# Optimization experiments

Hardware: AMD Instinct MI355X
Metric: run time of the kernel (lower is better)

## Reference

```python
import jax, jax.numpy as jnp
import numpy as np

B, N, D, DIM = 64, 512, 128, 128
NEG_INF = -1e9


def setup_inputs() -> dict:
    key = jax.random.key(0)
    k1, k2, k3, k4 = jax.random.split(key, 4)
    atom_query = jax.random.normal(k1, (B, N, D), dtype=jnp.float32)
    # binary atom-presence mask, broadcastable over feature dim
    mask = jax.random.randint(k2, (B, N, 1), 0, 2).astype(jnp.float32)
    s = 1.0 / np.sqrt(D)
    Wq = jax.random.normal(k3, (D, DIM), dtype=jnp.float32) * s
    Wk = jax.random.normal(k4, (D, DIM), dtype=jnp.float32) * s
    bq = jnp.zeros((DIM,), dtype=jnp.float32)
    bk = jnp.zeros((DIM,), dtype=jnp.float32)
    return {"atom_query": atom_query, "mask": mask, "Wq": Wq, "bq": bq, "Wk": Wk, "bk": bk}


def reference(atom_query, mask, Wq, bq, Wk, bk):
    # projections
    q = atom_query @ Wq + bq              # [B, N, dim]
    k = atom_query @ Wk + bk              # [B, N, dim]
    mq = mask * q                          # masked query
    mk = mask * k                          # masked key

    # energy[b,i,j] = mk[b,i] . mq[b,j], with diagonal zeroed, then summed over j.
    # sum_j energy[b,i,j] = mk[b,i] . (sum_j mq[b,j]) - mk[b,i] . mq[b,i]
    # (identical math to materializing the [B,N,N] energy and reducing)
    q_sum = mq.sum(axis=1)                                   # [B, dim]
    agg = jnp.einsum('bnd,bd->bn', mk, q_sum) - (mk * mq).sum(-1)  # [B, N]
    agg = agg[:, :, None] * mask                             # [B, N, 1]

    # euclidean normalize over atom axis (tf.linalg.normalize, axis=1)
    nrm = jnp.sqrt(jnp.sum(agg * agg, axis=1, keepdims=True))
    agg = agg / nrm

    # masked softmax over atoms
    agg = agg + (1.0 - mask) * NEG_INF
    attn = jax.nn.softmax(agg, axis=1)                       # [B, N, 1]

    # v_proj=False, kq_proj=True -> values are the key projection
    context = jnp.sum(mask * attn * k, axis=1)               # [B, dim]
    return attn, context
```

## Files before the change

kernel.cpp:

```cpp
#include <hip/hip_runtime.h>
#include <math.h>

#define NB 64
#define NN 512
#define ND 128

typedef __attribute__((ext_vector_type(8))) short short8;
typedef __attribute__((ext_vector_type(4))) float f32x4;

#define KVB_OFF   0
#define QK_OFF    (NB*NN*ND/2)
#define QSUMP_OFF (QK_OFF + NB*NN)

__device__ inline unsigned short f2bf(float x) {
    unsigned int u = __float_as_uint(x);
    return (unsigned short)((u + 0x7FFFu + ((u >> 16) & 1u)) >> 16);
}
__device__ inline float bf2f(unsigned short u) {
    return __uint_as_float(((unsigned int)u) << 16);
}

__global__ __launch_bounds__(256, 1) void proj_mfma(
    const float* __restrict__ aq, const float* __restrict__ mask,
    const float* __restrict__ Wq, const float* __restrict__ bq,
    const float* __restrict__ Wk, const float* __restrict__ bk,
    unsigned short* __restrict__ kvb, float* __restrict__ qk,
    float* __restrict__ qsum_part)
{
    __shared__ __align__(16) unsigned char sbuf[34816];
    unsigned short (*wst)[132] = (unsigned short (*)[132])sbuf;
    unsigned short (*ast)[136] = (unsigned short (*)[136])sbuf;
    __shared__ float mask_lds[128];
    __shared__ float qk_part[4][128];

    const int b    = blockIdx.x >> 2;
    const int m0   = (blockIdx.x & 3) << 7;
    const int t    = threadIdx.x;
    const int w    = t >> 6, lane = t & 63;
    const int quad = lane >> 4, l16 = lane & 15;

    short8 bfr[4][4];

    #pragma unroll
    for (int s = 0; s < 2; s++) {
        const float* Wsrc = s ? Wk : Wq;
        if (s) __syncthreads();
        {
            const float4* src = (const float4*)Wsrc;
            #pragma unroll
            for (int i = 0; i < 16; i++) {
                const int idx = t + 256*i;
                const int row = idx >> 5, c4 = idx & 31;
                const float4 v = src[idx];
                ushort4 o;
                o.x = f2bf(v.x); o.y = f2bf(v.y); o.z = f2bf(v.z); o.w = f2bf(v.w);
                *(ushort4*)&wst[row][c4*4] = o;
            }
        }
        __syncthreads();
        #pragma unroll
        for (int nt = 0; nt < 2; nt++) {
            const int col = w*32 + nt*16 + l16;
            #pragma unroll
            for (int kc = 0; kc < 4; kc++) {
                short8 v;
                #pragma unroll
                for (int j = 0; j < 8; j++)
                    v[j] = (short)wst[kc*32 + quad*8 + j][col];
                bfr[s*2 + nt][kc] = v;
            }
        }
    }
    __syncthreads();

    {
        const float4* src = (const float4*)(aq + ((size_t)b*NN + m0)*ND);
        #pragma unroll
        for (int i = 0; i < 16; i++) {
            const int idx = t + 256*i;
            const int row = idx >> 5, c4 = idx & 31;
            const float4 v = src[idx];
            ushort4 o;
            o.x = f2bf(v.x); o.y = f2bf(v.y); o.z = f2bf(v.z); o.w = f2bf(v.w);
            *(ushort4*)&ast[row][c4*4] = o;
        }
        if (t < 128) mask_lds[t] = mask[b*NN + m0 + t];
    }
    __syncthreads();

    f32x4 acc[8][4];
    #pragma unroll
    for (int m = 0; m < 8; m++)
        #pragma unroll
        for (int nt = 0; nt < 4; nt++)
            acc[m][nt] = (f32x4){0.f, 0.f, 0.f, 0.f};

    #pragma unroll
    for (int m = 0; m < 8; m++) {
        short8 afr[4];
        #pragma unroll
        for (int kc = 0; kc < 4; kc++)
            afr[kc] = *(const short8*)&ast[m*16 + l16][kc*32 + quad*8];
        #pragma unroll
        for (int nt = 0; nt < 4; nt++)
            #pragma unroll
            for (int kc = 0; kc < 4; kc++)
                acc[m][nt] = __builtin_amdgcn_mfma_f32_16x16x32_bf16(
                    afr[kc], bfr[nt][kc], acc[m][nt], 0, 0, 0);
    }

    float bv[4];
    #pragma unroll
    for (int nt = 0; nt < 2; nt++) bv[nt] = bq[w*32 + nt*16 + l16];
    #pragma unroll
    for (int nt = 2; nt < 4; nt++) bv[nt] = bk[w*32 + (nt-2)*16 + l16];
    #pragma unroll
    for (int m = 0; m < 8; m++)
        #pragma unroll
        for (int nt = 0; nt < 4; nt++)
            #pragma unroll
            for (int r = 0; r < 4; r++)
                acc[m][nt][r] += bv[nt];

    #pragma unroll
    for (int m = 0; m < 8; m++)
        #pragma unroll
        for (int r = 0; r < 4; r++) {
            const size_t row = (size_t)b*NN + m0 + m*16 + quad*4 + r;
            kvb[row*ND + w*32 + l16]      = f2bf(acc[m][2][r]);
            kvb[row*ND + w*32 + 16 + l16] = f2bf(acc[m][3][r]);
        }

    #pragma unroll
    for (int m = 0; m < 8; m++) {
        float p[4];
        #pragma unroll
        for (int r = 0; r < 4; r++)
            p[r] = acc[m][0][r]*acc[m][2][r] + acc[m][1][r]*acc[m][3][r];
        #pragma unroll
        for (int off = 1; off <= 8; off <<= 1)
            #pragma unroll
            for (int r = 0; r < 4; r++)
                p[r] += __shfl_xor(p[r], off);
        if (l16 == 0)
            #pragma unroll
            for (int r = 0; r < 4; r++)
                qk_part[w][m*16 + quad*4 + r] = p[r];
    }

    {
        float s0 = 0.f, s1 = 0.f;
        #pragma unroll
        for (int m = 0; m < 8; m++)
            #pragma unroll
            for (int r = 0; r < 4; r++) {
                const float mk = mask_lds[m*16 + quad*4 + r];
                s0 += mk * acc[m][0][r];
                s1 += mk * acc[m][1][r];
            }
        s0 += __shfl_xor(s0, 16); s0 += __shfl_xor(s0, 32);
        s1 += __shfl_xor(s1, 16); s1 += __shfl_xor(s1, 32);
        if (quad == 0) {
            const int slot = blockIdx.x * ND;
            qsum_part[slot + w*32 + l16]      = s0;
            qsum_part[slot + w*32 + 16 + l16] = s1;
        }
    }

    __syncthreads();
    if (t < 128)
        qk[(size_t)b*NN + m0 + t] =
            qk_part[0][t] + qk_part[1][t] + qk_part[2][t] + qk_part[3][t];
}

__global__ __launch_bounds__(512) void fused_attn(
    const float* __restrict__ mask, const unsigned short* __restrict__ kvb,
    const float* __restrict__ qk, const float* __restrict__ qsum_part,
    float* __restrict__ out_attn, float* __restrict__ out_ctx)
{
    __shared__ float qs[128];
    __shared__ float mask_s[512];
    __shared__ float agg_s[512];
    __shared__ float red[16];
    __shared__ float bc2[2];
    __shared__ float zred[8];
    __shared__ float zbc;
    __shared__ float ctx_part[32][33];

    const int b  = blockIdx.x >> 2;
    const int cg = blockIdx.x & 3;
    const int t = threadIdx.x, w = t >> 6, lane = t & 63;
    const size_t rowbase = (size_t)b * NN;

    if (t < 128)
        qs[t] = qsum_part[(b*4 + 0)*ND + t] + qsum_part[(b*4 + 1)*ND + t]
              + qsum_part[(b*4 + 2)*ND + t] + qsum_part[(b*4 + 3)*ND + t];
    mask_s[t] = mask[rowbase + t];
    __syncthreads();

    const int h = lane & 15, quad = lane >> 4;
    float qsf[8];
    #pragma unroll
    for (int j = 0; j < 8; j++) qsf[j] = qs[h*8 + j];

    for (int i0 = 0; i0 < 64; i0 += 4) {
        const int n = w*64 + i0 + quad;
        const short8 kr = *(const short8*)(kvb + (rowbase + n)*ND + h*8);
        float p = 0.f;
        #pragma unroll
        for (int j = 0; j < 8; j++)
            p += bf2f((unsigned short)kr[j]) * qsf[j];
        #pragma unroll
        for (int off = 1; off <= 8; off <<= 1) p += __shfl_xor(p, off);
        if (h == 0)
            agg_s[n] = mask_s[n] * (p - qk[rowbase + n]);
    }
    __syncthreads();

    const float v  = agg_s[t];
    const bool um  = mask_s[t] != 0.f;
    float sq = v * v;
    float mx = um ? v : -3.0e38f;
    #pragma unroll
    for (int off = 1; off <= 32; off <<= 1) {
        sq += __shfl_xor(sq, off);
        mx = fmaxf(mx, __shfl_xor(mx, off));
    }
    if (lane == 0) { red[w] = sq; red[8 + w] = mx; }
    __syncthreads();
    if (t == 0) {
        float s = 0.f, m = -3.0e38f;
        #pragma unroll
        for (int i = 0; i < 8; i++) { s += red[i]; m = fmaxf(m, red[8 + i]); }
        bc2[0] = sqrtf(s);
        bc2[1] = m;
    }
    __syncthreads();
    const float nrm = bc2[0];
    const float M   = bc2[1];

    const float e = um ? expf((v - M) / nrm) : 0.f;
    float z = e;
    #pragma unroll
    for (int off = 1; off <= 32; off <<= 1) z += __shfl_xor(z, off);
    if (lane == 0) zred[w] = z;
    agg_s[t] = e;
    __syncthreads();
    if (t == 0) {
        float s = 0.f;
        #pragma unroll
        for (int i = 0; i < 8; i++) s += zred[i];
        zbc = s;
    }
    __syncthreads();
    const float Z = zbc;
    if (cg == 0) out_attn[rowbase + t] = e / Z;

    const int c2  = (t & 15) * 2;
    const int col = cg*32 + c2;
    const int rg  = t >> 4;
    float a0 = 0.f, a1 = 0.f;
    for (int n = rg; n < NN; n += 32) {
        const ushort2 kk = *(const ushort2*)(kvb + (rowbase + n)*ND + col);
        const float ev = agg_s[n];
        a0 += ev * bf2f(kk.x);
        a1 += ev * bf2f(kk.y);
    }
    ctx_part[rg][c2]     = a0;
    ctx_part[rg][c2 + 1] = a1;
    __syncthreads();
    if (t < 32) {
        float s = 0.f;
        #pragma unroll
        for (int i = 0; i < 32; i++) s += ctx_part[i][t];
        out_ctx[(size_t)b*ND + cg*32 + t] = s / Z;
    }
}

extern "C" void kernel_launch(void* const* d_in, const int* in_sizes, int n_in,
                              void* d_out, int out_size, void* d_ws, size_t ws_size,
                              hipStream_t stream)
{
    const float* aq   = (const float*)d_in[0];
    const float* mask = (const float*)d_in[1];
    const float* Wq   = (const float*)d_in[2];
    const float* bq   = (const float*)d_in[3];
    const float* Wk   = (const float*)d_in[4];
    const float* bk   = (const float*)d_in[5];

    float* ws = (float*)d_ws;
    unsigned short* kvb       = (unsigned short*)(ws + KVB_OFF);
    float*          qk        = ws + QK_OFF;
    float*          qsum_part = ws + QSUMP_OFF;

    float* out_attn = (float*)d_out;
    float* out_ctx  = (float*)d_out + NB*NN;

    proj_mfma<<<dim3(256), dim3(256), 0, stream>>>(aq, mask, Wq, bq, Wk, bk,
                                                   kvb, qk, qsum_part);
    fused_attn<<<dim3(256), dim3(512), 0, stream>>>(mask, kvb, qk, qsum_part,
                                                    out_attn, out_ctx);
}
```

Measured before the change: 96.88 us.

## Fuse projection and attention into one per-batch kernel keeping K in LDS

Merges the two kernels into a single kernel with one 512-thread block per batch. The block projects the batch's atoms in 32-row chunks with a register prefetch of the next chunk, keeps the bf16 key projection in shared memory, and then runs the normalize, softmax and context reduction on-chip. This removes the workspace round trip for K, qk and the partial query sums, plus the second launch. The cost is a grid of only 64 blocks on a GPU with many more compute units, so each batch is processed serially inside one block with a sync-heavy chunk loop.

```diff
diff --git a/kernel.cpp b/kernel.cpp
--- a/kernel.cpp
+++ b/kernel.cpp
@@ -8,10 +8,6 @@
 typedef __attribute__((ext_vector_type(8))) short short8;
 typedef __attribute__((ext_vector_type(4))) float f32x4;
 
-#define KVB_OFF   0
-#define QK_OFF    (NB*NN*ND/2)
-#define QSUMP_OFF (QK_OFF + NB*NN)
-
 __device__ inline unsigned short f2bf(float x) {
     unsigned int u = __float_as_uint(x);
     return (unsigned short)((u + 0x7FFFu + ((u >> 16) & 1u)) >> 16);
@@ -20,200 +16,191 @@
     return __uint_as_float(((unsigned int)u) << 16);
 }
 
-__global__ __launch_bounds__(256, 1) void proj_mfma(
+__global__ __launch_bounds__(512, 1) void ga_one(
     const float* __restrict__ aq, const float* __restrict__ mask,
     const float* __restrict__ Wq, const float* __restrict__ bq,
     const float* __restrict__ Wk, const float* __restrict__ bk,
-    unsigned short* __restrict__ kvb, float* __restrict__ qk,
-    float* __restrict__ qsum_part)
+    float* __restrict__ out_attn, float* __restrict__ out_ctx)
 {
-    __shared__ __align__(16) unsigned char sbuf[34816];
-    unsigned short (*wst)[132] = (unsigned short (*)[132])sbuf;
-    unsigned short (*ast)[136] = (unsigned short (*)[136])sbuf;
-    __shared__ float mask_lds[128];
-    __shared__ float qk_part[4][128];
-
-    const int b    = blockIdx.x >> 2;
-    const int m0   = (blockIdx.x & 3) << 7;
+    __shared__ __align__(16) unsigned char kv_raw[512 * 136 * 2];
+    __shared__ __align__(16) unsigned char ab_raw[32 * 136 * 2];
+    __shared__ float mask_s[512];
+    __shared__ float agg_s[512];
+    __shared__ float qkp[4][512];
+    __shared__ float qs[128];
+    __shared__ float red2[16];
+    __shared__ float bcast[4];
+
+    unsigned short (*kv)[136]  = (unsigned short (*)[136])kv_raw;
+    unsigned short (*wst)[268] = (unsigned short (*)[268])kv_raw;
+    unsigned short (*ab)[136]  = (unsigned short (*)[136])ab_raw;
+    float (*ctx_part)[128]     = (float (*)[128])ab_raw;
+
+    const int b    = blockIdx.x;
     const int t    = threadIdx.x;
     const int w    = t >> 6, lane = t & 63;
     const int quad = lane >> 4, l16 = lane & 15;
-
-    short8 bfr[4][4];
-
-    #pragma unroll
-    for (int s = 0; s < 2; s++) {
-        const float* Wsrc = s ? Wk : Wq;
-        if (s) __syncthreads();
-        {
-            const float4* src = (const float4*)Wsrc;
-            #pragma unroll
-            for (int i = 0; i < 16; i++) {
-                const int idx = t + 256*i;
-                const int row = idx >> 5, c4 = idx & 31;
-                const float4 v = src[idx];
-                ushort4 o;
-                o.x = f2bf(v.x); o.y = f2bf(v.y); o.z = f2bf(v.z); o.w = f2bf(v.w);
-                *(ushort4*)&wst[row][c4*4] = o;
-            }
-        }
-        __syncthreads();
-        #pragma unroll
-        for (int nt = 0; nt < 2; nt++) {
-            const int col = w*32 + nt*16 + l16;
+    const bool isq = (w < 4);
+    const int cb   = (w & 3) * 32;
+
+    {
+        const float4* srcq = (const float4*)Wq;
+        const float4* srck = (const float4*)Wk;
+        #pragma unroll
+        for (int i = 0; i < 8; i++) {
+            const int idx = t + 512*i;
+            const int k = idx >> 5, c4 = idx & 31;
+            float4 v = srcq[idx];
+            ushort4 o;
+            o.x = f2bf(v.x); o.y = f2bf(v.y); o.z = f2bf(v.z); o.w = f2bf(v.w);
+            *(ushort4*)&wst[k][c4*4] = o;
+            v = srck[idx];
+            o.x = f2bf(v.x); o.y = f2bf(v.y); o.z = f2bf(v.z); o.w = f2bf(v.w);
+            *(ushort4*)&wst[k][128 + c4*4] = o;
+        }
+        mask_s[t] = mask[(size_t)b*NN + t];
+    }
+    __syncthreads();
+
+    short8 bfr[2][4];
+    {
+        const int colbase = cb + (isq ? 0 : 128);
+        #pragma unroll
+        for (int nt = 0; nt < 2; nt++)
             #pragma unroll
             for (int kc = 0; kc < 4; kc++) {
                 short8 v;
                 #pragma unroll
                 for (int j = 0; j < 8; j++)
-                    v[j] = (short)wst[kc*32 + quad*8 + j][col];
-                bfr[s*2 + nt][kc] = v;
+                    v[j] = (short)wst[kc*32 + quad*8 + j][colbase + nt*16 + l16];
+                bfr[nt][kc] = v;
             }
-        }
-    }
-    __syncthreads();
-
-    {
-        const float4* src = (const float4*)(aq + ((size_t)b*NN + m0)*ND);
-        #pragma unroll
-        for (int i = 0; i < 16; i++) {
-            const int idx = t + 256*i;
-            const int row = idx >> 5, c4 = idx & 31;
-            const float4 v = src[idx];
+    }
+    float bv[2];
+    #pragma unroll
+    for (int nt = 0; nt < 2; nt++)
+        bv[nt] = isq ? bq[cb + nt*16 + l16] : bk[cb + nt*16 + l16];
+    __syncthreads();
+
+    float s0 = 0.f, s1 = 0.f;
+
+    float4 pre0, pre1;
+    {
+        const float4* asrc = (const float4*)(aq + (size_t)b*NN*ND);
+        pre0 = asrc[t]; pre1 = asrc[t + 512];
+    }
+
+    for (int sc = 0; sc < 16; sc++) {
+        {
+            int idx = t, row = idx >> 5, c4 = idx & 31;
             ushort4 o;
-            o.x = f2bf(v.x); o.y = f2bf(v.y); o.z = f2bf(v.z); o.w = f2bf(v.w);
-            *(ushort4*)&ast[row][c4*4] = o;
-        }
-        if (t < 128) mask_lds[t] = mask[b*NN + m0 + t];
-    }
-    __syncthreads();
-
-    f32x4 acc[8][4];
-    #pragma unroll
-    for (int m = 0; m < 8; m++)
-        #pragma unroll
-        for (int nt = 0; nt < 4; nt++)
-            acc[m][nt] = (f32x4){0.f, 0.f, 0.f, 0.f};
-
-    #pragma unroll
-    for (int m = 0; m < 8; m++) {
-        short8 afr[4];
-        #pragma unroll
-        for (int kc = 0; kc < 4; kc++)
-            afr[kc] = *(const short8*)&ast[m*16 + l16][kc*32 + quad*8];
-        #pragma unroll
-        for (int nt = 0; nt < 4; nt++)
+            o.x = f2bf(pre0.x); o.y = f2bf(pre0.y); o.z = f2bf(pre0.z); o.w = f2bf(pre0.w);
+            *(ushort4*)&ab[row][c4*4] = o;
+            idx = t + 512; row = idx >> 5; c4 = idx & 31;
+            o.x = f2bf(pre1.x); o.y = f2bf(pre1.y); o.z = f2bf(pre1.z); o.w = f2bf(pre1.w);
+            *(ushort4*)&ab[row][c4*4] = o;
+        }
+        __syncthreads();
+        if (sc < 15) {
+            const float4* asrc = (const float4*)(aq + ((size_t)b*NN + (sc+1)*32)*ND);
+            pre0 = asrc[t]; pre1 = asrc[t + 512];
+        }
+
+        f32x4 acc[2][2];
+        #pragma unroll
+        for (int m = 0; m < 2; m++)
+            #pragma unroll
+            for (int nt = 0; nt < 2; nt++)
+                acc[m][nt] = (f32x4){0.f, 0.f, 0.f, 0.f};
+
+        #pragma unroll
+        for (int m = 0; m < 2; m++) {
+            short8 afr[4];
             #pragma unroll
             for (int kc = 0; kc < 4; kc++)
-                acc[m][nt] = __builtin_amdgcn_mfma_f32_16x16x32_bf16(
-                    afr[kc], bfr[nt][kc], acc[m][nt], 0, 0, 0);
-    }
-
-    float bv[4];
-    #pragma unroll
-    for (int nt = 0; nt < 2; nt++) bv[nt] = bq[w*32 + nt*16 + l16];
-    #pragma unroll
-    for (int nt = 2; nt < 4; nt++) bv[nt] = bk[w*32 + (nt-2)*16 + l16];
-    #pragma unroll
-    for (int m = 0; m < 8; m++)
-        #pragma unroll
-        for (int nt = 0; nt < 4; nt++)
-            #pragma unroll
-            for (int r = 0; r < 4; r++)
-                acc[m][nt][r] += bv[nt];
-
-    #pragma unroll
-    for (int m = 0; m < 8; m++)
-        #pragma unroll
-        for (int r = 0; r < 4; r++) {
-            const size_t row = (size_t)b*NN + m0 + m*16 + quad*4 + r;
-            kvb[row*ND + w*32 + l16]      = f2bf(acc[m][2][r]);
-            kvb[row*ND + w*32 + 16 + l16] = f2bf(acc[m][3][r]);
-        }
-
-    #pragma unroll
-    for (int m = 0; m < 8; m++) {
-        float p[4];
-        #pragma unroll
-        for (int r = 0; r < 4; r++)
-            p[r] = acc[m][0][r]*acc[m][2][r] + acc[m][1][r]*acc[m][3][r];
-        #pragma unroll
-        for (int off = 1; off <= 8; off <<= 1)
-            #pragma unroll
-            for (int r = 0; r < 4; r++)
-                p[r] += __shfl_xor(p[r], off);
-        if (l16 == 0)
-            #pragma unroll
-            for (int r = 0; r < 4; r++)
-                qk_part[w][m*16 + quad*4 + r] = p[r];
-    }
-
-    {
-        float s0 = 0.f, s1 = 0.f;
-        #pragma unroll
-        for (int m = 0; m < 8; m++)
-            #pragma unroll
-            for (int r = 0; r < 4; r++) {
-                const float mk = mask_lds[m*16 + quad*4 + r];
-                s0 += mk * acc[m][0][r];
-                s1 += mk * acc[m][1][r];
+                afr[kc] = *(const short8*)&ab[m*16 + l16][kc*32 + quad*8];
+            #pragma unroll
+            for (int nt = 0; nt < 2; nt++)
+                #pragma unroll
+                for (int kc = 0; kc < 4; kc++)
+                    acc[m][nt] = __builtin_amdgcn_mfma_f32_16x16x32_bf16(
+                        afr[kc], bfr[nt][kc], acc[m][nt], 0, 0, 0);
+        }
+        #pragma unroll
+        for (int m = 0; m < 2; m++)
+            #pragma unroll
+            for (int nt = 0; nt < 2; nt++)
+                #pragma unroll
+                for (int r = 0; r < 4; r++)
+                    acc[m][nt][r] += bv[nt];
+
+        if (!isq) {
+            #pragma unroll
+            for (int m = 0; m < 2; m++)
+                #pragma unroll
+                for (int r = 0; r < 4; r++) {
+                    const int row = sc*32 + m*16 + quad*4 + r;
+                    kv[row][cb + l16]      = f2bf(acc[m][0][r]);
+                    kv[row][cb + 16 + l16] = f2bf(acc[m][1][r]);
+                }
+        }
+        __syncthreads();
+
+        if (isq) {
+            #pragma unroll
+            for (int m = 0; m < 2; m++) {
+                float p[4];
+                #pragma unroll
+                for (int r = 0; r < 4; r++) {
+                    const int row = sc*32 + m*16 + quad*4 + r;
+                    p[r] = acc[m][0][r]*bf2f(kv[row][cb + l16])
+                         + acc[m][1][r]*bf2f(kv[row][cb + 16 + l16]);
+                }
+                #pragma unroll
+                for (int off = 1; off <= 8; off <<= 1)
+                    #pragma unroll
+                    for (int r = 0; r < 4; r++)
+                        p[r] += __shfl_xor(p[r], off);
+                if (l16 == 0)
+                    #pragma unroll
+                    for (int r = 0; r < 4; r++)
+                        qkp[w][sc*32 + m*16 + quad*4 + r] = p[r];
+                #pragma unroll
+                for (int r = 0; r < 4; r++) {
+                    const int row = sc*32 + m*16 + quad*4 + r;
+                    const float mk = mask_s[row];
+                    s0 += mk * acc[m][0][r];
+                    s1 += mk * acc[m][1][r];
+                }
             }
+        }
+    }
+
+    if (isq) {
         s0 += __shfl_xor(s0, 16); s0 += __shfl_xor(s0, 32);
         s1 += __shfl_xor(s1, 16); s1 += __shfl_xor(s1, 32);
-        if (quad == 0) {
-            const int slot = blockIdx.x * ND;
-            qsum_part[slot + w*32 + l16]      = s0;
-            qsum_part[slot + w*32 + 16 + l16] = s1;
-        }
-    }
-
-    __syncthreads();
-    if (t < 128)
-        qk[(size_t)b*NN + m0 + t] =
-            qk_part[0][t] + qk_part[1][t] + qk_part[2][t] + qk_part[3][t];
-}
-
-__global__ __launch_bounds__(512) void fused_attn(
-    const float* __restrict__ mask, const unsigned short* __restrict__ kvb,
-    const float* __restrict__ qk, const float* __restrict__ qsum_part,
-    float* __restrict__ out_attn, float* __restrict__ out_ctx)
-{
-    __shared__ float qs[128];
-    __shared__ float mask_s[512];
-    __shared__ float agg_s[512];
-    __shared__ float red[16];
-    __shared__ float bc2[2];
-    __shared__ float zred[8];
-    __shared__ float zbc;
-    __shared__ float ctx_part[32][33];
-
-    const int b  = blockIdx.x >> 2;
-    const int cg = blockIdx.x & 3;
-    const int t = threadIdx.x, w = t >> 6, lane = t & 63;
-    const size_t rowbase = (size_t)b * NN;
-
-    if (t < 128)
-        qs[t] = qsum_part[(b*4 + 0)*ND + t] + qsum_part[(b*4 + 1)*ND + t]
-              + qsum_part[(b*4 + 2)*ND + t] + qsum_part[(b*4 + 3)*ND + t];
-    mask_s[t] = mask[rowbase + t];
-    __syncthreads();
-
-    const int h = lane & 15, quad = lane >> 4;
-    float qsf[8];
-    #pragma unroll
-    for (int j = 0; j < 8; j++) qsf[j] = qs[h*8 + j];
-
-    for (int i0 = 0; i0 < 64; i0 += 4) {
-        const int n = w*64 + i0 + quad;
-        const short8 kr = *(const short8*)(kvb + (rowbase + n)*ND + h*8);
-        float p = 0.f;
-        #pragma unroll
-        for (int j = 0; j < 8; j++)
-            p += bf2f((unsigned short)kr[j]) * qsf[j];
-        #pragma unroll
-        for (int off = 1; off <= 8; off <<= 1) p += __shfl_xor(p, off);
-        if (h == 0)
-            agg_s[n] = mask_s[n] * (p - qk[rowbase + n]);
+        if (lane < 16) { qs[cb + lane] = s0; qs[cb + 16 + lane] = s1; }
+    }
+    __syncthreads();
+
+    {
+        float qsf[8];
+        #pragma unroll
+        for (int j = 0; j < 8; j++) qsf[j] = qs[l16*8 + j];
+        for (int i0 = 0; i0 < 64; i0 += 4) {
+            const int n = w*64 + i0 + quad;
+            const short8 kr = *(const short8*)&kv[n][l16*8];
+            float p = 0.f;
+            #pragma unroll
+            for (int j = 0; j < 8; j++)
+                p += bf2f((unsigned short)kr[j]) * qsf[j];
+            #pragma unroll
+            for (int off = 1; off <= 8; off <<= 1) p += __shfl_xor(p, off);
+            if (l16 == 0) {
+                const float qkv = qkp[0][n] + qkp[1][n] + qkp[2][n] + qkp[3][n];
+                agg_s[n] = mask_s[n] * (p - qkv);
+            }
+        }
     }
     __syncthreads();
 
@@ -226,55 +213,45 @@
         sq += __shfl_xor(sq, off);
         mx = fmaxf(mx, __shfl_xor(mx, off));
     }
-    if (lane == 0) { red[w] = sq; red[8 + w] = mx; }
+    if (lane == 0) { red2[w] = sq; red2[8 + w] = mx; }
     __syncthreads();
     if (t == 0) {
         float s = 0.f, m = -3.0e38f;
         #pragma unroll
-        for (int i = 0; i < 8; i++) { s += red[i]; m = fmaxf(m, red[8 + i]); }
-        bc2[0] = sqrtf(s);
-        bc2[1] = m;
-    }
-    __syncthreads();
-    const float nrm = bc2[0];
-    const float M   = bc2[1];
+        for (int i = 0; i < 8; i++) { s += red2[i]; m = fmaxf(m, red2[8 + i]); }
+        bcast[0] = sqrtf(s);
+        bcast[1] = m;
+    }
+    __syncthreads();
+    const float nrm = bcast[0];
+    const float M   = bcast[1];
 
     const float e = um ? expf((v - M) / nrm) : 0.f;
+    agg_s[t] = e;
     float z = e;
     #pragma unroll
     for (int off = 1; off <= 32; off <<= 1) z += __shfl_xor(z, off);
-    if (lane == 0) zred[w] = z;
-    agg_s[t] = e;
+    if (lane == 0) red2[w] = z;
     __syncthreads();
     if (t == 0) {
         float s = 0.f;
         #pragma unroll
-        for (int i = 0; i < 8; i++) s += zred[i];
-        zbc = s;
-    }
-    __syncthreads();
-    const float Z = zbc;
-    if (cg == 0) out_attn[rowbase + t] = e / Z;
-
-    const int c2  = (t & 15) * 2;
-    const int col = cg*32 + c2;
-    const int rg  = t >> 4;
-    float a0 = 0.f, a1 = 0.f;
-    for (int n = rg; n < NN; n += 32) {
-        const ushort2 kk = *(const ushort2*)(kvb + (rowbase + n)*ND + col);
-        const float ev = agg_s[n];
-        a0 += ev * bf2f(kk.x);
-        a1 += ev * bf2f(kk.y);
-    }
-    ctx_part[rg][c2]     = a0;
-    ctx_part[rg][c2 + 1] = a1;
-    __syncthreads();
-    if (t < 32) {
-        float s = 0.f;
-        #pragma unroll
-        for (int i = 0; i < 32; i++) s += ctx_part[i][t];
-        out_ctx[(size_t)b*ND + cg*32 + t] = s / Z;
-    }
+        for (int i = 0; i < 8; i++) s += red2[i];
+        bcast[2] = s;
+    }
+    __syncthreads();
+    const float Z = bcast[2];
+    out_attn[(size_t)b*NN + t] = e / Z;
+
+    const int col = t & 127, g = t >> 7;
+    float a = 0.f;
+    for (int n = g; n < NN; n += 4)
+        a += agg_s[n] * bf2f(kv[n][col]);
+    ctx_part[g][col] = a;
+    __syncthreads();
+    if (t < 128)
+        out_ctx[(size_t)b*ND + t] =
+            (ctx_part[0][t] + ctx_part[1][t] + ctx_part[2][t] + ctx_part[3][t]) / Z;
 }
 
 extern "C" void kernel_launch(void* const* d_in, const int* in_sizes, int n_in,
@@ -288,16 +265,9 @@
     const float* Wk   = (const float*)d_in[4];
     const float* bk   = (const float*)d_in[5];
 
-    float* ws = (float*)d_ws;
-    unsigned short* kvb       = (unsigned short*)(ws + KVB_OFF);
-    float*          qk        = ws + QK_OFF;
-    float*          qsum_part = ws + QSUMP_OFF;
-
     float* out_attn = (float*)d_out;
     float* out_ctx  = (float*)d_out + NB*NN;
 
-    proj_mfma<<<dim3(256), dim3(256), 0, stream>>>(aq, mask, Wq, bq, Wk, bk,
-                                                   kvb, qk, qsum_part);
-    fused_attn<<<dim3(256), dim3(512), 0, stream>>>(mask, kvb, qk, qsum_part,
-                                                    out_attn, out_ctx);
-}
+    ga_one<<<dim3(NB), dim3(512), 0, stream>>>(aq, mask, Wq, bq, Wk, bk,
+                                               out_attn, out_ctx);
+}
```

Measured after the change: 104.4 us. 7.7% more time.

## Fuse projection and attention kernels with per-batch inter-block flag sync

Applied to the files above, without the earlier changes.

Merges the projection kernel and the attention kernel into a single 256-block launch. The four blocks of each batch signal completion through release-stored flags in workspace and spin-wait on each other before running the normalize, softmax and context stage with 256 threads. Block indices are remapped so the four blocks of a batch land on the same XCD, which should keep the shared kvb data in one L2. This removes the second launch and the gap between kernels, but it needs all blocks to be resident at once. The flags are never reset, so on a later call the waits can pass before the other blocks of the batch have written their data.

```diff
diff --git a/kernel.cpp b/kernel.cpp
--- a/kernel.cpp
+++ b/kernel.cpp
@@ -4,6 +4,7 @@
 #define NB 64
 #define NN 512
 #define ND 128
+#define DONE_FLAG 0x1234ABCDu
 
 typedef __attribute__((ext_vector_type(8))) short short8;
 typedef __attribute__((ext_vector_type(4))) float f32x4;
@@ -11,6 +12,7 @@
 #define KVB_OFF   0
 #define QK_OFF    (NB*NN*ND/2)
 #define QSUMP_OFF (QK_OFF + NB*NN)
+#define FLAG_OFF  (QSUMP_OFF + NB*4*ND)
 
 __device__ inline unsigned short f2bf(float x) {
     unsigned int u = __float_as_uint(x);
@@ -20,27 +22,40 @@
     return __uint_as_float(((unsigned int)u) << 16);
 }
 
-__global__ __launch_bounds__(256, 1) void proj_mfma(
+__global__ __launch_bounds__(256, 1) void ga_fused(
     const float* __restrict__ aq, const float* __restrict__ mask,
     const float* __restrict__ Wq, const float* __restrict__ bq,
     const float* __restrict__ Wk, const float* __restrict__ bk,
     unsigned short* __restrict__ kvb, float* __restrict__ qk,
-    float* __restrict__ qsum_part)
+    float* __restrict__ qsum_part, unsigned int* __restrict__ flags,
+    float* __restrict__ out_attn, float* __restrict__ out_ctx)
 {
     __shared__ __align__(16) unsigned char sbuf[34816];
     unsigned short (*wst)[132] = (unsigned short (*)[132])sbuf;
     unsigned short (*ast)[136] = (unsigned short (*)[136])sbuf;
     __shared__ float mask_lds[128];
     __shared__ float qk_part[4][128];
-
-    const int b    = blockIdx.x >> 2;
-    const int m0   = (blockIdx.x & 3) << 7;
+    __shared__ float qs[128];
+    __shared__ float mask_s[512];
+    __shared__ float agg_s[512];
+    __shared__ float red[8];
+    __shared__ float bc2[2];
+    __shared__ float zred[4];
+    __shared__ float zbc;
+    __shared__ float ctx_part[16][33];
+
+    const int p    = blockIdx.x;
+    const int xcd  = p & 7, slot = p >> 3;
+    const int b    = ((slot >> 2) << 3) | xcd;
+    const int c    = slot & 3;
+    const int lb   = b*4 + c;
+    const int m0   = c << 7;
+
     const int t    = threadIdx.x;
     const int w    = t >> 6, lane = t & 63;
     const int quad = lane >> 4, l16 = lane & 15;
 
     short8 bfr[4][4];
-
     #pragma unroll
     for (int s = 0; s < 2; s++) {
         const float* Wsrc = s ? Wk : Wq;
@@ -133,19 +148,19 @@
 
     #pragma unroll
     for (int m = 0; m < 8; m++) {
-        float p[4];
+        float pr[4];
         #pragma unroll
         for (int r = 0; r < 4; r++)
-            p[r] = acc[m][0][r]*acc[m][2][r] + acc[m][1][r]*acc[m][3][r];
+            pr[r] = acc[m][0][r]*acc[m][2][r] + acc[m][1][r]*acc[m][3][r];
         #pragma unroll
         for (int off = 1; off <= 8; off <<= 1)
             #pragma unroll
             for (int r = 0; r < 4; r++)
-                p[r] += __shfl_xor(p[r], off);
+                pr[r] += __shfl_xor(pr[r], off);
         if (l16 == 0)
             #pragma unroll
             for (int r = 0; r < 4; r++)
-                qk_part[w][m*16 + quad*4 + r] = p[r];
+                qk_part[w][m*16 + quad*4 + r] = pr[r];
     }
 
     {
@@ -161,9 +176,9 @@
         s0 += __shfl_xor(s0, 16); s0 += __shfl_xor(s0, 32);
         s1 += __shfl_xor(s1, 16); s1 += __shfl_xor(s1, 32);
         if (quad == 0) {
-            const int slot = blockIdx.x * ND;
-            qsum_part[slot + w*32 + l16]      = s0;
-            qsum_part[slot + w*32 + 16 + l16] = s1;
+            const int slotq = lb * ND;
+            qsum_part[slotq + w*32 + l16]      = s0;
+            qsum_part[slotq + w*32 + 16 + l16] = s1;
         }
     }
 
@@ -171,67 +186,64 @@
     if (t < 128)
         qk[(size_t)b*NN + m0 + t] =
             qk_part[0][t] + qk_part[1][t] + qk_part[2][t] + qk_part[3][t];
-}
-
-__global__ __launch_bounds__(512) void fused_attn(
-    const float* __restrict__ mask, const unsigned short* __restrict__ kvb,
-    const float* __restrict__ qk, const float* __restrict__ qsum_part,
-    float* __restrict__ out_attn, float* __restrict__ out_ctx)
-{
-    __shared__ float qs[128];
-    __shared__ float mask_s[512];
-    __shared__ float agg_s[512];
-    __shared__ float red[16];
-    __shared__ float bc2[2];
-    __shared__ float zred[8];
-    __shared__ float zbc;
-    __shared__ float ctx_part[32][33];
-
-    const int b  = blockIdx.x >> 2;
-    const int cg = blockIdx.x & 3;
-    const int t = threadIdx.x, w = t >> 6, lane = t & 63;
+
+    __syncthreads();
+    __threadfence();
+    if (t == 0)
+        __hip_atomic_store(&flags[lb], DONE_FLAG, __ATOMIC_RELEASE,
+                           __HIP_MEMORY_SCOPE_AGENT);
+    if (t < 4) {
+        while (__hip_atomic_load(&flags[b*4 + t], __ATOMIC_RELAXED,
+                                 __HIP_MEMORY_SCOPE_AGENT) != DONE_FLAG)
+            __builtin_amdgcn_s_sleep(2);
+    }
+    __syncthreads();
+    __threadfence();
+
+    const int cg = c;
     const size_t rowbase = (size_t)b * NN;
 
     if (t < 128)
         qs[t] = qsum_part[(b*4 + 0)*ND + t] + qsum_part[(b*4 + 1)*ND + t]
               + qsum_part[(b*4 + 2)*ND + t] + qsum_part[(b*4 + 3)*ND + t];
-    mask_s[t] = mask[rowbase + t];
-    __syncthreads();
-
-    const int h = lane & 15, quad = lane >> 4;
-    float qsf[8];
-    #pragma unroll
-    for (int j = 0; j < 8; j++) qsf[j] = qs[h*8 + j];
-
-    for (int i0 = 0; i0 < 64; i0 += 4) {
-        const int n = w*64 + i0 + quad;
-        const short8 kr = *(const short8*)(kvb + (rowbase + n)*ND + h*8);
-        float p = 0.f;
-        #pragma unroll
-        for (int j = 0; j < 8; j++)
-            p += bf2f((unsigned short)kr[j]) * qsf[j];
-        #pragma unroll
-        for (int off = 1; off <= 8; off <<= 1) p += __shfl_xor(p, off);
-        if (h == 0)
-            agg_s[n] = mask_s[n] * (p - qk[rowbase + n]);
-    }
-    __syncthreads();
-
-    const float v  = agg_s[t];
-    const bool um  = mask_s[t] != 0.f;
-    float sq = v * v;
-    float mx = um ? v : -3.0e38f;
+    mask_s[t]       = mask[rowbase + t];
+    mask_s[t + 256] = mask[rowbase + t + 256];
+    __syncthreads();
+
+    {
+        float qsf[8];
+        #pragma unroll
+        for (int j = 0; j < 8; j++) qsf[j] = qs[l16*8 + j];
+        for (int i0 = 0; i0 < 128; i0 += 4) {
+            const int n = w*128 + i0 + quad;
+            const short8 kr = *(const short8*)(kvb + (rowbase + n)*ND + l16*8);
+            float pp = 0.f;
+            #pragma unroll
+            for (int j = 0; j < 8; j++)
+                pp += bf2f((unsigned short)kr[j]) * qsf[j];
+            #pragma unroll
+            for (int off = 1; off <= 8; off <<= 1) pp += __shfl_xor(pp, off);
+            if (l16 == 0)
+                agg_s[n] = mask_s[n] * (pp - qk[rowbase + n]);
+        }
+    }
+    __syncthreads();
+
+    const float v0 = agg_s[t], v1 = agg_s[t + 256];
+    const bool um0 = mask_s[t] != 0.f, um1 = mask_s[t + 256] != 0.f;
+    float sq = v0*v0 + v1*v1;
+    float mx = fmaxf(um0 ? v0 : -3.0e38f, um1 ? v1 : -3.0e38f);
     #pragma unroll
     for (int off = 1; off <= 32; off <<= 1) {
         sq += __shfl_xor(sq, off);
         mx = fmaxf(mx, __shfl_xor(mx, off));
     }
-    if (lane == 0) { red[w] = sq; red[8 + w] = mx; }
+    if (lane == 0) { red[w] = sq; red[4 + w] = mx; }
     __syncthreads();
     if (t == 0) {
         float s = 0.f, m = -3.0e38f;
         #pragma unroll
-        for (int i = 0; i < 8; i++) { s += red[i]; m = fmaxf(m, red[8 + i]); }
+        for (int i = 0; i < 4; i++) { s += red[i]; m = fmaxf(m, red[4 + i]); }
         bc2[0] = sqrtf(s);
         bc2[1] = m;
     }
@@ -239,28 +251,28 @@
     const float nrm = bc2[0];
     const float M   = bc2[1];
 
-    const float e = um ? expf((v - M) / nrm) : 0.f;
-    float z = e;
+    const float e0 = um0 ? expf((v0 - M) / nrm) : 0.f;
+    const float e1 = um1 ? expf((v1 - M) / nrm) : 0.f;
+    float z = e0 + e1;
     #pragma unroll
     for (int off = 1; off <= 32; off <<= 1) z += __shfl_xor(z, off);
     if (lane == 0) zred[w] = z;
-    agg_s[t] = e;
-    __syncthreads();
-    if (t == 0) {
-        float s = 0.f;
-        #pragma unroll
-        for (int i = 0; i < 8; i++) s += zred[i];
-        zbc = s;
-    }
+    agg_s[t] = e0;
+    agg_s[t + 256] = e1;
+    __syncthreads();
+    if (t == 0) zbc = zred[0] + zred[1] + zred[2] + zred[3];
     __syncthreads();
     const float Z = zbc;
-    if (cg == 0) out_attn[rowbase + t] = e / Z;
+    if (cg == 0) {
+        out_attn[rowbase + t]       = e0 / Z;
+        out_attn[rowbase + t + 256] = e1 / Z;
+    }
 
     const int c2  = (t & 15) * 2;
     const int col = cg*32 + c2;
     const int rg  = t >> 4;
     float a0 = 0.f, a1 = 0.f;
-    for (int n = rg; n < NN; n += 32) {
+    for (int n = rg; n < NN; n += 16) {
         const ushort2 kk = *(const ushort2*)(kvb + (rowbase + n)*ND + col);
         const float ev = agg_s[n];
         a0 += ev * bf2f(kk.x);
@@ -272,7 +284,7 @@
     if (t < 32) {
         float s = 0.f;
         #pragma unroll
-        for (int i = 0; i < 32; i++) s += ctx_part[i][t];
+        for (int i = 0; i < 16; i++) s += ctx_part[i][t];
         out_ctx[(size_t)b*ND + cg*32 + t] = s / Z;
     }
 }
@@ -292,12 +304,12 @@
     unsigned short* kvb       = (unsigned short*)(ws + KVB_OFF);
     float*          qk        = ws + QK_OFF;
     float*          qsum_part = ws + QSUMP_OFF;
+    unsigned int*   flags     = (unsigned int*)(ws + FLAG_OFF);
 
     float* out_attn = (float*)d_out;
     float* out_ctx  = (float*)d_out + NB*NN;
 
-    proj_mfma<<<dim3(256), dim3(256), 0, stream>>>(aq, mask, Wq, bq, Wk, bk,
-                                                   kvb, qk, qsum_part);
-    fused_attn<<<dim3(256), dim3(512), 0, stream>>>(mask, kvb, qk, qsum_part,
-                                                    out_attn, out_ctx);
+    ga_fused<<<dim3(256), dim3(256), 0, stream>>>(aq, mask, Wq, bq, Wk, bk,
+                                                  kvb, qk, qsum_part, flags,
+                                                  out_attn, out_ctx);
 }
```

Result: slower. 134.1 us (+38.5%).

## Split projection output columns into two halves to double grid parallelism

Applied to the files above, without the earlier changes.

The projection kernel now runs 512 blocks instead of 256. Each block computes half of the output columns (64 of 128) for both Q and K, so it loads only half of each weight matrix and keeps half the accumulators. Partial q·k dot products and q-sum partials are written per column half and combined in the attention kernel. The aim is better CU occupancy (launch bounds raised to 2 blocks per CU, fewer registers) at the cost of converting each activation tile to bf16 twice, plus extra partial-sum traffic.

```diff
diff --git a/kernel.cpp b/kernel.cpp
--- a/kernel.cpp
+++ b/kernel.cpp
@@ -9,8 +9,8 @@
 typedef __attribute__((ext_vector_type(4))) float f32x4;
 
 #define KVB_OFF   0
-#define QK_OFF    (NB*NN*ND/2)
-#define QSUMP_OFF (QK_OFF + NB*NN)
+#define QKH_OFF   (NB*NN*ND/2)
+#define QSUMP_OFF (QKH_OFF + NB*2*NN)
 
 __device__ inline unsigned short f2bf(float x) {
     unsigned int u = __float_as_uint(x);
@@ -20,58 +20,46 @@
     return __uint_as_float(((unsigned int)u) << 16);
 }
 
-__global__ __launch_bounds__(256, 1) void proj_mfma(
+__global__ __launch_bounds__(256, 2) void proj_mfma(
     const float* __restrict__ aq, const float* __restrict__ mask,
     const float* __restrict__ Wq, const float* __restrict__ bq,
     const float* __restrict__ Wk, const float* __restrict__ bk,
-    unsigned short* __restrict__ kvb, float* __restrict__ qk,
+    unsigned short* __restrict__ kvb, float* __restrict__ qkh,
     float* __restrict__ qsum_part)
 {
-    __shared__ __align__(16) unsigned char sbuf[34816];
-    unsigned short (*wst)[132] = (unsigned short (*)[132])sbuf;
-    unsigned short (*ast)[136] = (unsigned short (*)[136])sbuf;
+    __shared__ __align__(16) unsigned short wst[128][132];
+    __shared__ __align__(16) unsigned short ast[128][136];
     __shared__ float mask_lds[128];
     __shared__ float qk_part[4][128];
 
-    const int b    = blockIdx.x >> 2;
-    const int m0   = (blockIdx.x & 3) << 7;
+    const int p    = blockIdx.x;
+    const int h    = p >> 8;
+    const int rem  = p & 255;
+    const int b    = rem >> 2;
+    const int rc   = rem & 3;
+    const int m0   = rc << 7;
+
     const int t    = threadIdx.x;
     const int w    = t >> 6, lane = t & 63;
     const int quad = lane >> 4, l16 = lane & 15;
 
-    short8 bfr[4][4];
-
-    #pragma unroll
-    for (int s = 0; s < 2; s++) {
-        const float* Wsrc = s ? Wk : Wq;
-        if (s) __syncthreads();
-        {
-            const float4* src = (const float4*)Wsrc;
-            #pragma unroll
-            for (int i = 0; i < 16; i++) {
-                const int idx = t + 256*i;
-                const int row = idx >> 5, c4 = idx & 31;
-                const float4 v = src[idx];
-                ushort4 o;
-                o.x = f2bf(v.x); o.y = f2bf(v.y); o.z = f2bf(v.z); o.w = f2bf(v.w);
-                *(ushort4*)&wst[row][c4*4] = o;
-            }
-        }
-        __syncthreads();
-        #pragma unroll
-        for (int nt = 0; nt < 2; nt++) {
-            const int col = w*32 + nt*16 + l16;
-            #pragma unroll
-            for (int kc = 0; kc < 4; kc++) {
-                short8 v;
-                #pragma unroll
-                for (int j = 0; j < 8; j++)
-                    v[j] = (short)wst[kc*32 + quad*8 + j][col];
-                bfr[s*2 + nt][kc] = v;
-            }
-        }
-    }
-    __syncthreads();
+    {
+        const float4* srcq = (const float4*)Wq;
+        const float4* srck = (const float4*)Wk;
+        #pragma unroll
+        for (int i = 0; i < 8; i++) {
+            const int idx = t + 256*i;
+            const int row = idx >> 4, c4 = idx & 15;
+            const int gidx = row*32 + h*16 + c4;
+            float4 v = srcq[gidx];
+            ushort4 o;
+            o.x = f2bf(v.x); o.y = f2bf(v.y); o.z = f2bf(v.z); o.w = f2bf(v.w);
+            *(ushort4*)&wst[row][c4*4] = o;
+            v = srck[gidx];
+            o.x = f2bf(v.x); o.y = f2bf(v.y); o.z = f2bf(v.z); o.w = f2bf(v.w);
+            *(ushort4*)&wst[row][64 + c4*4] = o;
+        }
+    }
 
     {
         const float4* src = (const float4*)(aq + ((size_t)b*NN + m0)*ND);
@@ -88,12 +76,30 @@
     }
     __syncthreads();
 
-    f32x4 acc[8][4];
-    #pragma unroll
-    for (int m = 0; m < 8; m++)
-        #pragma unroll
-        for (int nt = 0; nt < 4; nt++)
-            acc[m][nt] = (f32x4){0.f, 0.f, 0.f, 0.f};
+    short8 bfr[2][4];
+    {
+        const int colq = w*16 + l16;
+        #pragma unroll
+        for (int kc = 0; kc < 4; kc++) {
+            short8 vq, vk;
+            #pragma unroll
+            for (int j = 0; j < 8; j++) {
+                vq[j] = (short)wst[kc*32 + quad*8 + j][colq];
+                vk[j] = (short)wst[kc*32 + quad*8 + j][64 + colq];
+            }
+            bfr[0][kc] = vq;
+            bfr[1][kc] = vk;
+        }
+    }
+    const float bvq = bq[h*64 + w*16 + l16];
+    const float bvk = bk[h*64 + w*16 + l16];
+
+    f32x4 acc[8][2];
+    #pragma unroll
+    for (int m = 0; m < 8; m++) {
+        acc[m][0] = (f32x4){0.f, 0.f, 0.f, 0.f};
+        acc[m][1] = (f32x4){0.f, 0.f, 0.f, 0.f};
+    }
 
     #pragma unroll
     for (int m = 0; m < 8; m++) {
@@ -102,80 +108,71 @@
         for (int kc = 0; kc < 4; kc++)
             afr[kc] = *(const short8*)&ast[m*16 + l16][kc*32 + quad*8];
         #pragma unroll
-        for (int nt = 0; nt < 4; nt++)
-            #pragma unroll
-            for (int kc = 0; kc < 4; kc++)
-                acc[m][nt] = __builtin_amdgcn_mfma_f32_16x16x32_bf16(
-                    afr[kc], bfr[nt][kc], acc[m][nt], 0, 0, 0);
-    }
-
-    float bv[4];
-    #pragma unroll
-    for (int nt = 0; nt < 2; nt++) bv[nt] = bq[w*32 + nt*16 + l16];
-    #pragma unroll
-    for (int nt = 2; nt < 4; nt++) bv[nt] = bk[w*32 + (nt-2)*16 + l16];
+        for (int kc = 0; kc < 4; kc++) {
+            acc[m][0] = __builtin_amdgcn_mfma_f32_16x16x32_bf16(
+                afr[kc], bfr[0][kc], acc[m][0], 0, 0, 0);
+            acc[m][1] = __builtin_amdgcn_mfma_f32_16x16x32_bf16(
+                afr[kc], bfr[1][kc], acc[m][1], 0, 0, 0);
+        }
+    }
+
     #pragma unroll
     for (int m = 0; m < 8; m++)
         #pragma unroll
-        for (int nt = 0; nt < 4; nt++)
+        for (int r = 0; r < 4; r++) {
+            acc[m][0][r] += bvq;
+            acc[m][1][r] += bvk;
+        }
+
+    {
+        const int col = h*64 + w*16 + l16;
+        #pragma unroll
+        for (int m = 0; m < 8; m++)
+            #pragma unroll
+            for (int r = 0; r < 4; r++) {
+                const size_t row = (size_t)b*NN + m0 + m*16 + quad*4 + r;
+                kvb[row*ND + col] = f2bf(acc[m][1][r]);
+            }
+    }
+
+    #pragma unroll
+    for (int m = 0; m < 8; m++) {
+        float pr[4];
+        #pragma unroll
+        for (int r = 0; r < 4; r++)
+            pr[r] = acc[m][0][r] * acc[m][1][r];
+        #pragma unroll
+        for (int off = 1; off <= 8; off <<= 1)
             #pragma unroll
             for (int r = 0; r < 4; r++)
-                acc[m][nt][r] += bv[nt];
-
-    #pragma unroll
-    for (int m = 0; m < 8; m++)
-        #pragma unroll
-        for (int r = 0; r < 4; r++) {
-            const size_t row = (size_t)b*NN + m0 + m*16 + quad*4 + r;
-            kvb[row*ND + w*32 + l16]      = f2bf(acc[m][2][r]);
-            kvb[row*ND + w*32 + 16 + l16] = f2bf(acc[m][3][r]);
-        }
-
-    #pragma unroll
-    for (int m = 0; m < 8; m++) {
-        float p[4];
-        #pragma unroll
-        for (int r = 0; r < 4; r++)
-            p[r] = acc[m][0][r]*acc[m][2][r] + acc[m][1][r]*acc[m][3][r];
-        #pragma unroll
-        for (int off = 1; off <= 8; off <<= 1)
+                pr[r] += __shfl_xor(pr[r], off);
+        if (l16 == 0)
             #pragma unroll
             for (int r = 0; r < 4; r++)
-                p[r] += __shfl_xor(p[r], off);
-        if (l16 == 0)
+                qk_part[w][m*16 + quad*4 + r] = pr[r];
+    }
+
+    {
+        float s0 = 0.f;
+        #pragma unroll
+        for (int m = 0; m < 8; m++)
             #pragma unroll
             for (int r = 0; r < 4; r++)
-                qk_part[w][m*16 + quad*4 + r] = p[r];
-    }
-
-    {
-        float s0 = 0.f, s1 = 0.f;
-        #pragma unroll
-        for (int m = 0; m < 8; m++)
-            #pragma unroll
-            for (int r = 0; r < 4; r++) {
-                const float mk = mask_lds[m*16 + quad*4 + r];
-                s0 += mk * acc[m][0][r];
-                s1 += mk * acc[m][1][r];
-            }
+                s0 += mask_lds[m*16 + quad*4 + r] * acc[m][0][r];
         s0 += __shfl_xor(s0, 16); s0 += __shfl_xor(s0, 32);
-        s1 += __shfl_xor(s1, 16); s1 += __shfl_xor(s1, 32);
-        if (quad == 0) {
-            const int slot = blockIdx.x * ND;
-            qsum_part[slot + w*32 + l16]      = s0;
-            qsum_part[slot + w*32 + 16 + l16] = s1;
-        }
+        if (quad == 0)
+            qsum_part[(b*8 + rc*2 + h)*64 + w*16 + l16] = s0;
     }
 
     __syncthreads();
     if (t < 128)
-        qk[(size_t)b*NN + m0 + t] =
+        qkh[((size_t)b*2 + h)*NN + m0 + t] =
             qk_part[0][t] + qk_part[1][t] + qk_part[2][t] + qk_part[3][t];
 }
 
 __global__ __launch_bounds__(512) void fused_attn(
     const float* __restrict__ mask, const unsigned short* __restrict__ kvb,
-    const float* __restrict__ qk, const float* __restrict__ qsum_part,
+    const float* __restrict__ qkh, const float* __restrict__ qsum_part,
     float* __restrict__ out_attn, float* __restrict__ out_ctx)
 {
     __shared__ float qs[128];
@@ -192,28 +189,35 @@
     const int t = threadIdx.x, w = t >> 6, lane = t & 63;
     const size_t rowbase = (size_t)b * NN;
 
-    if (t < 128)
-        qs[t] = qsum_part[(b*4 + 0)*ND + t] + qsum_part[(b*4 + 1)*ND + t]
-              + qsum_part[(b*4 + 2)*ND + t] + qsum_part[(b*4 + 3)*ND + t];
+    if (t < 128) {
+        const int hh = t >> 6, cc = t & 63;
+        qs[t] = qsum_part[(b*8 + 0*2 + hh)*64 + cc]
+              + qsum_part[(b*8 + 1*2 + hh)*64 + cc]
+              + qsum_part[(b*8 + 2*2 + hh)*64 + cc]
+              + qsum_part[(b*8 + 3*2 + hh)*64 + cc];
+    }
     mask_s[t] = mask[rowbase + t];
     __syncthreads();
 
-    const int h = lane & 15, quad = lane >> 4;
+    const int h16 = lane & 15, quad = lane >> 4;
     float qsf[8];
     #pragma unroll
-    for (int j = 0; j < 8; j++) qsf[j] = qs[h*8 + j];
+    for (int j = 0; j < 8; j++) qsf[j] = qs[h16*8 + j];
 
     for (int i0 = 0; i0 < 64; i0 += 4) {
         const int n = w*64 + i0 + quad;
-        const short8 kr = *(const short8*)(kvb + (rowbase + n)*ND + h*8);
-        float p = 0.f;
+        const short8 kr = *(const short8*)(kvb + (rowbase + n)*ND + h16*8);
+        float pp = 0.f;
         #pragma unroll
         for (int j = 0; j < 8; j++)
-            p += bf2f((unsigned short)kr[j]) * qsf[j];
-        #pragma unroll
-        for (int off = 1; off <= 8; off <<= 1) p += __shfl_xor(p, off);
-        if (h == 0)
-            agg_s[n] = mask_s[n] * (p - qk[rowbase + n]);
+            pp += bf2f((unsigned short)kr[j]) * qsf[j];
+        #pragma unroll
+        for (int off = 1; off <= 8; off <<= 1) pp += __shfl_xor(pp, off);
+        if (h16 == 0) {
+            const float qkv = qkh[((size_t)b*2 + 0)*NN + n]
+                            + qkh[((size_t)b*2 + 1)*NN + n];
+            agg_s[n] = mask_s[n] * (pp - qkv);
+        }
     }
     __syncthreads();
 
@@ -290,14 +294,14 @@
 
     float* ws = (float*)d_ws;
     unsigned short* kvb       = (unsigned short*)(ws + KVB_OFF);
-    float*          qk        = ws + QK_OFF;
+    float*          qkh       = ws + QKH_OFF;
     float*          qsum_part = ws + QSUMP_OFF;
 
     float* out_attn = (float*)d_out;
     float* out_ctx  = (float*)d_out + NB*NN;
 
-    proj_mfma<<<dim3(256), dim3(256), 0, stream>>>(aq, mask, Wq, bq, Wk, bk,
-                                                   kvb, qk, qsum_part);
-    fused_attn<<<dim3(256), dim3(512), 0, stream>>>(mask, kvb, qk, qsum_part,
+    proj_mfma<<<dim3(512), dim3(256), 0, stream>>>(aq, mask, Wq, bq, Wk, bk,
+                                                   kvb, qkh, qsum_part);
+    fused_attn<<<dim3(256), dim3(512), 0, stream>>>(mask, kvb, qkh, qsum_part,
                                                     out_attn, out_ctx);
 }
```

Result: no change. 97.91 us (+1.1%).
